# Optimization experiments

Hardware: AMD Instinct MI355X
Metric: run time of the kernel (lower is better)

Reference implementation:

```python
import jax, jax.numpy as jnp
import numpy as np

STD = 0.01

def setup_inputs() -> dict:
    key = jax.random.key(0)
    k1, k2, k3 = jax.random.split(key, 3)
    B, T, D = 16, 4096, 512
    x = jax.random.normal(k1, (B, T, D), dtype=jnp.float32)
    att_W = jax.random.normal(k2, (D, D), dtype=jnp.float32) * STD
    att_v = jax.random.normal(k3, (D,), dtype=jnp.float32) * STD
    return {"x": x, "att_W": att_W, "att_v": att_v}

def reference(x, att_W, att_v):
    # additive attention scores: tanh(x @ W) @ v -> [B, T]
    y = jnp.tanh(jnp.einsum('btd,de->bte', x, att_W))
    scores = jnp.einsum('btd,d->bt', y, att_v)
    weights = jax.nn.softmax(scores, axis=-1)          # softmax over sequence
    out = jnp.einsum('bt,btd->bd', weights, x)         # weighted sum pooling
    return out.astype(jnp.float32)
```

## Files before the change

kernel.cpp:

```cpp
#include <hip/hip_runtime.h>
#include <hip/hip_bf16.h>
#include <math.h>

#define BB 16
#define TT 4096
#define DD 512
#define MM (BB*TT)

typedef __bf16 bf16x8 __attribute__((ext_vector_type(8)));
typedef float  f32x4  __attribute__((ext_vector_type(4)));

__device__ inline unsigned short f2bf(float f) {
    unsigned u = __builtin_bit_cast(unsigned, f) + 0x8000u;
    return (unsigned short)(u >> 16);
}

__device__ inline unsigned pack_bf16x2(float lo, float hi) {
    unsigned u0 = __builtin_bit_cast(unsigned, lo) + 0x8000u;
    unsigned u1 = __builtin_bit_cast(unsigned, hi) + 0x8000u;
    return __builtin_amdgcn_perm(u1, u0, 0x07060302);
}

__device__ inline float tanh_fast(float y) {
    float e = __expf(2.0f * y);
    return 1.0f - 2.0f * __builtin_amdgcn_rcpf(e + 1.0f);
}

__global__ void wb_kernel(const float* __restrict__ W, unsigned short* __restrict__ Wb) {
    int u = blockIdx.x * 256 + threadIdx.x;
    int lane = u & 63;
    int fid  = u >> 6;
    int ni = fid & 1;
    int s  = (fid >> 1) & 15;
    int p  = (fid >> 5) & 7;
    int h  = fid >> 8;
    int n  = h * 256 + p * 32 + ni * 16 + (lane & 15);
    int k0 = s * 32 + (lane >> 4) * 8;
    unsigned short o[8];
    #pragma unroll
    for (int j = 0; j < 8; j++) o[j] = f2bf(W[(size_t)(k0 + j) * DD + n]);
    *(uint4*)(Wb + (size_t)u * 8) = *(uint4*)o;
}

__global__ __launch_bounds__(256, 2) void scorepool_kernel(
        const float* __restrict__ x, const unsigned short* __restrict__ Wb,
        const float* __restrict__ v,
        float* __restrict__ num_ws, float* __restrict__ mz_ws) {
    __shared__ unsigned short As[64 * DD];
    __shared__ float sbuf[2][64];
    __shared__ float ew[64];
    __shared__ float mzsh[2];
    __shared__ float psum[4][DD];

    const int tid  = threadIdx.x;
    const int m0   = blockIdx.x * 64;
    const int wid  = tid >> 6;
    const int lane = tid & 63;
    const int l15  = lane & 15;
    const int q    = lane >> 4;
    const int r3   = l15 & 7;
    const int wr   = (wid & 1) * 32;
    const int wh   = wid >> 1;

    #pragma unroll 4
    for (int i = 0; i < 16; i++) {
        int u = i * 256 + tid;
        int r = u >> 6;
        int c = u & 63;
        const float* gp = x + (size_t)(m0 + r) * DD + c * 8;
        float4 f0 = *(const float4*)(gp);
        float4 f1 = *(const float4*)(gp + 4);
        uint4 o;
        o.x = pack_bf16x2(f0.x, f0.y);
        o.y = pack_bf16x2(f0.z, f0.w);
        o.z = pack_bf16x2(f1.x, f1.y);
        o.w = pack_bf16x2(f1.z, f1.w);
        *(uint4*)(&As[r * DD + (c ^ (r & 7)) * 8]) = o;
    }

    const unsigned short* bqp = Wb + (size_t)wh * 131072 + lane * 8;
    bf16x8 b[4][2];
    #pragma unroll
    for (int g = 0; g < 3; g++) {
        b[g][0] = *(const bf16x8*)(bqp);
        b[g][1] = *(const bf16x8*)(bqp + 512);
        bqp += 1024;
    }

    __syncthreads();

    float vpart[2][4];
    #pragma unroll
    for (int mi = 0; mi < 2; mi++)
        #pragma unroll
        for (int rr = 0; rr < 4; rr++)
            vpart[mi][rr] = 0.f;

#define A_FRAG(mi, s) (*(const bf16x8*)(&As[(wr + (mi)*16 + l15) * DD + ((((s)*4 + q) ^ r3) * 8)]))

    bf16x8 a[2][2];
    a[0][0] = A_FRAG(0, 0);
    a[0][1] = A_FRAG(1, 0);

    #pragma unroll 1
    for (int p = 0; p < 8; p++) {
        f32x4 acc[2][2];
        #pragma unroll
        for (int mi = 0; mi < 2; mi++)
            #pragma unroll
            for (int ni = 0; ni < 2; ni++)
                acc[mi][ni] = (f32x4){0.f, 0.f, 0.f, 0.f};

        #pragma unroll
        for (int s = 0; s < 16; s++) {
            const int cur = s & 1;
            const int ns  = (s + 1) & 15;
            a[cur ^ 1][0] = A_FRAG(0, ns);
            a[cur ^ 1][1] = A_FRAG(1, ns);
            b[(s + 3) & 3][0] = *(const bf16x8*)(bqp);
            b[(s + 3) & 3][1] = *(const bf16x8*)(bqp + 512);
            bqp += 1024;
            #pragma unroll
            for (int mi = 0; mi < 2; mi++)
                #pragma unroll
                for (int ni = 0; ni < 2; ni++)
                    acc[mi][ni] = __builtin_amdgcn_mfma_f32_16x16x32_bf16(
                        a[cur][mi], b[s & 3][ni], acc[mi][ni], 0, 0, 0);
        }

        float vv0 = v[wh * 256 + p * 32 + l15];
        float vv1 = v[wh * 256 + p * 32 + 16 + l15];
        #pragma unroll
        for (int mi = 0; mi < 2; mi++)
            #pragma unroll
            for (int rr = 0; rr < 4; rr++)
                vpart[mi][rr] += tanh_fast(acc[mi][0][rr]) * vv0
                               + tanh_fast(acc[mi][1][rr]) * vv1;
    }
#undef A_FRAG

    #pragma unroll
    for (int mi = 0; mi < 2; mi++)
        #pragma unroll
        for (int rr = 0; rr < 4; rr++) {
            float sum = vpart[mi][rr];
            sum += __shfl_xor(sum, 1);
            sum += __shfl_xor(sum, 2);
            sum += __shfl_xor(sum, 4);
            sum += __shfl_xor(sum, 8);
            if (l15 == 0)
                sbuf[wh][wr + mi * 16 + q * 4 + rr] = sum;
        }
    __syncthreads();

    if (tid < 64) {
        float s = sbuf[0][tid] + sbuf[1][tid];
        float m = s;
        #pragma unroll
        for (int off = 32; off; off >>= 1) m = fmaxf(m, __shfl_xor(m, off));
        float e = __expf(s - m);
        float z = e;
        #pragma unroll
        for (int off = 32; off; off >>= 1) z += __shfl_xor(z, off);
        ew[tid] = e;
        if (tid == 0) { mzsh[0] = m; mzsh[1] = z; }
    }
    __syncthreads();

    const int cx = tid & 63;
    const int rg = tid >> 6;
    float nacc[8];
    #pragma unroll
    for (int j = 0; j < 8; j++) nacc[j] = 0.f;
    #pragma unroll 4
    for (int i = 0; i < 16; i++) {
        int r = rg * 16 + i;
        uint4 u = *(const uint4*)(&As[r * DD + ((cx ^ (r & 7)) * 8)]);
        float e = ew[r];
        nacc[0] += e * __builtin_bit_cast(float, u.x << 16);
        nacc[1] += e * __builtin_bit_cast(float, u.x & 0xFFFF0000u);
        nacc[2] += e * __builtin_bit_cast(float, u.y << 16);
        nacc[3] += e * __builtin_bit_cast(float, u.y & 0xFFFF0000u);
        nacc[4] += e * __builtin_bit_cast(float, u.z << 16);
        nacc[5] += e * __builtin_bit_cast(float, u.z & 0xFFFF0000u);
        nacc[6] += e * __builtin_bit_cast(float, u.w << 16);
        nacc[7] += e * __builtin_bit_cast(float, u.w & 0xFFFF0000u);
    }
    *(float4*)(&psum[rg][cx * 8])     = *(float4*)(&nacc[0]);
    *(float4*)(&psum[rg][cx * 8 + 4]) = *(float4*)(&nacc[4]);
    __syncthreads();

    if (tid < 128) {
        int c = tid * 4;
        f32x4 f = *(const f32x4*)(&psum[0][c]);
        f += *(const f32x4*)(&psum[1][c]);
        f += *(const f32x4*)(&psum[2][c]);
        f += *(const f32x4*)(&psum[3][c]);
        *(f32x4*)(num_ws + (size_t)blockIdx.x * DD + c) = f;
    }
    if (tid == 0) {
        mz_ws[2 * blockIdx.x]     = mzsh[0];
        mz_ws[2 * blockIdx.x + 1] = mzsh[1];
    }
}

__global__ void combine_kernel(const float* __restrict__ num_ws,
                               const float* __restrict__ mz_ws,
                               float* __restrict__ out) {
    __shared__ float fs[64];
    __shared__ float sinv_sh;
    const int b   = blockIdx.x;
    const int tid = threadIdx.x;

    if (tid < 64) {
        float m = mz_ws[(b * 64 + tid) * 2];
        float z = mz_ws[(b * 64 + tid) * 2 + 1];
        float M = m;
        #pragma unroll
        for (int off = 32; off; off >>= 1) M = fmaxf(M, __shfl_xor(M, off));
        float f  = __expf(m - M);
        float fz = f * z;
        #pragma unroll
        for (int off = 32; off; off >>= 1) fz += __shfl_xor(fz, off);
        fs[tid] = f;
        if (tid == 0) sinv_sh = 1.0f / fz;
    }
    __syncthreads();

    float a0 = 0.f, a1 = 0.f;
    #pragma unroll 4
    for (int c = 0; c < 64; c++) {
        float f = fs[c];
        const float* np = num_ws + (size_t)(b * 64 + c) * DD;
        a0 += f * np[tid];
        a1 += f * np[tid + 256];
    }
    const float sinv = sinv_sh;
    out[b * DD + tid]       = a0 * sinv;
    out[b * DD + tid + 256] = a1 * sinv;
}

extern "C" void kernel_launch(void* const* d_in, const int* in_sizes, int n_in,
                              void* d_out, int out_size, void* d_ws, size_t ws_size,
                              hipStream_t stream) {
    (void)in_sizes; (void)n_in; (void)out_size; (void)ws_size;
    const float* x = (const float*)d_in[0];
    const float* W = (const float*)d_in[1];
    const float* v = (const float*)d_in[2];
    float* out = (float*)d_out;

    unsigned short* Wb = (unsigned short*)d_ws;
    float* num_ws      = (float*)((char*)d_ws + 512 * 1024 + 8 * 1024);
    float* mz_ws       = (float*)((char*)d_ws + 512 * 1024 + 8 * 1024 + 2 * 1024 * 1024);

    wb_kernel<<<128, 256, 0, stream>>>(W, Wb);

    scorepool_kernel<<<MM / 64, 256, 0, stream>>>(x, Wb, v, num_ws, mz_ws);

    combine_kernel<<<BB, 256, 0, stream>>>(num_ws, mz_ws, out);
}
```

Before: 255.0 us.

## Repartition MFMA work so each wave covers all 64 rows and a quarter of columns

```diff
diff --git a/kernel.cpp b/kernel.cpp
--- a/kernel.cpp
+++ b/kernel.cpp
@@ -32,9 +32,9 @@
     int fid  = u >> 6;
     int ni = fid & 1;
     int s  = (fid >> 1) & 15;
-    int p  = (fid >> 5) & 7;
-    int h  = fid >> 8;
-    int n  = h * 256 + p * 32 + ni * 16 + (lane & 15);
+    int p  = (fid >> 5) & 3;
+    int qh = fid >> 7;
+    int n  = qh * 128 + p * 32 + ni * 16 + (lane & 15);
     int k0 = s * 32 + (lane >> 4) * 8;
     unsigned short o[8];
     #pragma unroll
@@ -47,20 +47,18 @@
         const float* __restrict__ v,
         float* __restrict__ num_ws, float* __restrict__ mz_ws) {
     __shared__ unsigned short As[64 * DD];
-    __shared__ float sbuf[2][64];
+    __shared__ float sbuf[4][64];
     __shared__ float ew[64];
     __shared__ float mzsh[2];
     __shared__ float psum[4][DD];
 
     const int tid  = threadIdx.x;
     const int m0   = blockIdx.x * 64;
-    const int wid  = tid >> 6;
+    const int qh   = tid >> 6;
     const int lane = tid & 63;
     const int l15  = lane & 15;
     const int q    = lane >> 4;
     const int r3   = l15 & 7;
-    const int wr   = (wid & 1) * 32;
-    const int wh   = wid >> 1;
 
     #pragma unroll 4
     for (int i = 0; i < 16; i++) {
@@ -78,69 +76,77 @@
         *(uint4*)(&As[r * DD + (c ^ (r & 7)) * 8]) = o;
     }
 
-    const unsigned short* bqp = Wb + (size_t)wh * 131072 + lane * 8;
-    bf16x8 b[4][2];
-    #pragma unroll
-    for (int g = 0; g < 3; g++) {
+    const unsigned short* bqp = Wb + (size_t)qh * 65536 + lane * 8;
+    bf16x8 b[8][2];
+    #pragma unroll
+    for (int g = 0; g < 7; g++) {
         b[g][0] = *(const bf16x8*)(bqp);
         b[g][1] = *(const bf16x8*)(bqp + 512);
         bqp += 1024;
     }
 
-    __syncthreads();
-
-    float vpart[2][4];
-    #pragma unroll
-    for (int mi = 0; mi < 2; mi++)
+    float vv[4][2];
+    #pragma unroll
+    for (int pp = 0; pp < 4; pp++) {
+        vv[pp][0] = v[qh * 128 + pp * 32 + l15];
+        vv[pp][1] = v[qh * 128 + pp * 32 + 16 + l15];
+    }
+
+    __syncthreads();
+
+    float vpart[4][4];
+    #pragma unroll
+    for (int mi = 0; mi < 4; mi++)
         #pragma unroll
         for (int rr = 0; rr < 4; rr++)
             vpart[mi][rr] = 0.f;
 
-#define A_FRAG(mi, s) (*(const bf16x8*)(&As[(wr + (mi)*16 + l15) * DD + ((((s)*4 + q) ^ r3) * 8)]))
-
-    bf16x8 a[2][2];
-    a[0][0] = A_FRAG(0, 0);
-    a[0][1] = A_FRAG(1, 0);
+#define A_FRAG(mi, s) (*(const bf16x8*)(&As[((mi) * 16 + l15) * DD + ((((s) * 4 + q) ^ r3) * 8)]))
+
+    bf16x8 a[4][4];
+    #pragma unroll
+    for (int mi = 0; mi < 4; mi++) {
+        a[0][mi] = A_FRAG(mi, 0);
+        a[1][mi] = A_FRAG(mi, 1);
+        a[2][mi] = A_FRAG(mi, 2);
+    }
 
     #pragma unroll 1
-    for (int p = 0; p < 8; p++) {
-        f32x4 acc[2][2];
-        #pragma unroll
-        for (int mi = 0; mi < 2; mi++)
+    for (int p = 0; p < 4; p++) {
+        f32x4 acc[4][2];
+        #pragma unroll
+        for (int mi = 0; mi < 4; mi++) {
+            acc[mi][0] = (f32x4){0.f, 0.f, 0.f, 0.f};
+            acc[mi][1] = (f32x4){0.f, 0.f, 0.f, 0.f};
+        }
+
+        #pragma unroll
+        for (int s = 0; s < 16; s++) {
+            const int ns = (s + 3) & 15;
             #pragma unroll
-            for (int ni = 0; ni < 2; ni++)
-                acc[mi][ni] = (f32x4){0.f, 0.f, 0.f, 0.f};
-
-        #pragma unroll
-        for (int s = 0; s < 16; s++) {
-            const int cur = s & 1;
-            const int ns  = (s + 1) & 15;
-            a[cur ^ 1][0] = A_FRAG(0, ns);
-            a[cur ^ 1][1] = A_FRAG(1, ns);
-            b[(s + 3) & 3][0] = *(const bf16x8*)(bqp);
-            b[(s + 3) & 3][1] = *(const bf16x8*)(bqp + 512);
+            for (int mi = 0; mi < 4; mi++) a[(s + 3) & 3][mi] = A_FRAG(mi, ns);
+            b[(s + 7) & 7][0] = *(const bf16x8*)(bqp);
+            b[(s + 7) & 7][1] = *(const bf16x8*)(bqp + 512);
             bqp += 1024;
             #pragma unroll
-            for (int mi = 0; mi < 2; mi++)
+            for (int mi = 0; mi < 4; mi++)
                 #pragma unroll
                 for (int ni = 0; ni < 2; ni++)
                     acc[mi][ni] = __builtin_amdgcn_mfma_f32_16x16x32_bf16(
-                        a[cur][mi], b[s & 3][ni], acc[mi][ni], 0, 0, 0);
+                        a[s & 3][mi], b[s & 7][ni], acc[mi][ni], 0, 0, 0);
         }
 
-        float vv0 = v[wh * 256 + p * 32 + l15];
-        float vv1 = v[wh * 256 + p * 32 + 16 + l15];
-        #pragma unroll
-        for (int mi = 0; mi < 2; mi++)
+        #pragma unroll
+        for (int mi = 0; mi < 4; mi++)
             #pragma unroll
             for (int rr = 0; rr < 4; rr++)
-                vpart[mi][rr] += tanh_fast(acc[mi][0][rr]) * vv0
-                               + tanh_fast(acc[mi][1][rr]) * vv1;
+                vpart[mi][rr] += tanh_fast(acc[mi][0][rr]) * vv[p][0]
+                               + tanh_fast(acc[mi][1][rr]) * vv[p][1];
     }
 #undef A_FRAG
 
     #pragma unroll
-    for (int mi = 0; mi < 2; mi++)
+    for (int mi = 0; mi < 4; mi++)
         #pragma unroll
         for (int rr = 0; rr < 4; rr++) {
             float sum = vpart[mi][rr];
@@ -149,16 +155,16 @@
             sum += __shfl_xor(sum, 4);
             sum += __shfl_xor(sum, 8);
             if (l15 == 0)
-                sbuf[wh][wr + mi * 16 + q * 4 + rr] = sum;
+                sbuf[qh][mi * 16 + q * 4 + rr] = sum;
         }
     __syncthreads();
 
     if (tid < 64) {
-        float s = sbuf[0][tid] + sbuf[1][tid];
-        float m = s;
+        float sc = sbuf[0][tid] + sbuf[1][tid] + sbuf[2][tid] + sbuf[3][tid];
+        float m = sc;
         #pragma unroll
         for (int off = 32; off; off >>= 1) m = fmaxf(m, __shfl_xor(m, off));
-        float e = __expf(s - m);
+        float e = __expf(sc - m);
         float z = e;
         #pragma unroll
         for (int off = 32; off; off >>= 1) z += __shfl_xor(z, off);
@@ -250,8 +256,8 @@
     float* out = (float*)d_out;
 
     unsigned short* Wb = (unsigned short*)d_ws;
-    float* num_ws      = (float*)((char*)d_ws + 512 * 1024 + 8 * 1024);
-    float* mz_ws       = (float*)((char*)d_ws + 512 * 1024 + 8 * 1024 + 2 * 1024 * 1024);
+    float* num_ws      = (float*)((char*)d_ws + 512 * 1024 + 16 * 1024);
+    float* mz_ws       = (float*)((char*)d_ws + 512 * 1024 + 16 * 1024 + 2 * 1024 * 1024);
 
     wb_kernel<<<128, 256, 0, stream>>>(W, Wb);
 
```

Result: slower. 330.8 us (+29.7%).
